# Kernel optimization log

Hardware: AMD Instinct MI355X
Metric: run time of the kernel (lower is better)

The kernel has to match this reference:

```python
import jax, jax.numpy as jnp
import numpy as np

N_TYPES = 4
N_PAIRS = N_TYPES * N_TYPES          # 16 (src_type, dst_type) pairs
N_GLOBAL_ET = 24                     # global edge event types
N_LOCAL_ET = 16                      # per-pair predictor output classes
D = 256                              # hidden dim
E = 262144                           # number of edges


def setup_inputs() -> dict:
    key = jax.random.key(0)
    ks = jax.random.split(key, 12)
    s = 0.05
    h_src = jax.random.normal(ks[0], (E, D), jnp.float32)
    h_dst = jax.random.normal(ks[1], (E, D), jnp.float32)
    src_type_idx = jax.random.randint(ks[2], (E,), 0, N_TYPES)
    dst_type_idx = jax.random.randint(ks[3], (E,), 0, N_TYPES)
    edge_type_classes = jax.random.randint(ks[4], (E,), 0, N_GLOBAL_ET)
    # decoder params: Linear(concat(h_src,h_dst)) -> D, split into two matrices
    W1 = jax.random.normal(ks[5], (D, D), jnp.float32) * s
    W2 = jax.random.normal(ks[6], (D, D), jnp.float32) * s
    b_dec = jnp.zeros((D,), jnp.float32)
    # per-(src,dst)-pair predictor heads, stacked
    W_pred = jax.random.normal(ks[7], (N_PAIRS, D, N_LOCAL_ET), jnp.float32) * s
    b_pred = jnp.zeros((N_PAIRS, N_LOCAL_ET), jnp.float32)
    # event_map[pair, global_edge_type] -> local class id
    event_map = jax.random.randint(ks[8], (N_PAIRS, N_GLOBAL_ET), 0, N_LOCAL_ET)
    return {
        'h_src': h_src, 'h_dst': h_dst,
        'W1': W1, 'W2': W2, 'b_dec': b_dec,
        'W_pred': W_pred, 'b_pred': b_pred,
        'src_type_idx': src_type_idx, 'dst_type_idx': dst_type_idx,
        'edge_type_classes': edge_type_classes, 'event_map': event_map,
        'inference': 0,
    }


def reference(h_src, h_dst, W1, W2, b_dec, W_pred, b_pred,
              src_type_idx, dst_type_idx, edge_type_classes, event_map,
              inference):
    # decoder: Linear(concat(h_src, h_dst)) -> D, ReLU
    h = jax.nn.relu(h_src @ W1 + h_dst @ W2 + b_dec)            # [E, D]
    pair = src_type_idx * N_TYPES + dst_type_idx                 # [E]
    # grouped per-pair linear heads: compute all heads, select per-edge head
    logits_all = jnp.einsum('ed,pdc->epc', h, W_pred) + b_pred   # [E, P, C]
    logits = jnp.take_along_axis(
        logits_all, pair[:, None, None], axis=1)[:, 0]           # [E, C]
    labels = event_map[pair, edge_type_classes]                  # [E]
    logp = jax.nn.log_softmax(logits, axis=-1)
    per_edge_loss = -jnp.take_along_axis(logp, labels[:, None], axis=1)[:, 0]
    # training path: per-group mean, then mean over non-empty groups
    sums = jax.ops.segment_sum(per_edge_loss, pair, num_segments=N_PAIRS)
    cnts = jax.ops.segment_sum(jnp.ones_like(per_edge_loss), pair,
                               num_segments=N_PAIRS)
    present = cnts > 0
    gmean = jnp.where(present, sums / jnp.maximum(cnts, 1.0), 0.0)
    loss = jnp.sum(gmean) / jnp.sum(present.astype(jnp.float32))
    return loss
```

## Files before the change

### kernel.cpp

```cpp
#include <hip/hip_runtime.h>
#include <stdint.h>

#define E_EDGES 262144
#define TILE_M 128
#define NBLK (E_EDGES / TILE_M)

typedef unsigned short ushort_t;
typedef __attribute__((ext_vector_type(8))) short short8;
typedef __attribute__((ext_vector_type(4))) float f32x4;

#define OFF_WT   0
#define OFF_WP   (512*256*2)
#define OFF_HIST (OFF_WP + 8*16*64*8*2)
#define OFF_SUMS (OFF_HIST + 64)

__device__ __forceinline__ ushort_t f2bf(float f) {
  union { float f; unsigned u; } c; c.f = f;
  unsigned r = c.u + 0x7fffu + ((c.u >> 16) & 1u);
  return (ushort_t)(r >> 16);
}

__device__ __forceinline__ void async_copy16(void* lds, const void* g) {
  __builtin_amdgcn_global_load_lds(
      (const __attribute__((address_space(1))) unsigned int*)g,
      (__attribute__((address_space(3))) unsigned int*)lds, 16, 0, 0);
}

__global__ __launch_bounds__(256) void prep_k(const float* __restrict__ W1,
    const float* __restrict__ W2, const float* __restrict__ Wp,
    char* __restrict__ ws) {
  const int i = blockIdx.x * 256 + threadIdx.x;
  if (i < 512 * 256) {
    ushort_t* Wt = (ushort_t*)(ws + OFF_WT);
    const int n = i >> 9, k = i & 511;
    const float v = (k < 256) ? W1[(k << 8) + n] : W2[((k - 256) << 8) + n];
    Wt[i] = f2bf(v);
  }
  if (i < 8 * 16 * 64 * 8) {
    ushort_t* Wpf = (ushort_t*)(ws + OFF_WP);
    const int jj = i & 7, l = (i >> 3) & 63, p = (i >> 9) & 15, s = i >> 13;
    const int k = s * 32 + (l >> 4) * 8 + jj, c = l & 15;
    Wpf[i] = f2bf(Wp[((p << 8) + k) * 16 + c]);
  }
  if (i < 16) {
    ((int*)(ws + OFF_HIST))[i] = 0;
    ((float*)(ws + OFF_SUMS))[i] = 0.f;
  }
}

__global__ __launch_bounds__(512, 4) void main_k(
    const float* __restrict__ h_src, const float* __restrict__ h_dst,
    const float* __restrict__ b_dec, const float* __restrict__ b_pred,
    const int* __restrict__ st, const int* __restrict__ dt,
    const int* __restrict__ etc_arr, const int* __restrict__ emap,
    char* __restrict__ ws) {
  const ushort_t* Wt = (const ushort_t*)(ws + OFF_WT);
  const short8* Wpf2 = (const short8*)(ws + OFF_WP);
  int* hist = (int*)(ws + OFF_HIST);
  float* sums = (float*)(ws + OFF_SUMS);

  const int tb = blockIdx.x * TILE_M;

  __shared__ __align__(16) char smem[65536];
  __shared__ float lsums[16];
  __shared__ int lcnts[16];
  ushort_t* A_buf0 = (ushort_t*)smem;
  ushort_t* A_buf1 = (ushort_t*)(smem + 10240);
  char* B_buf0 = smem + 20480;
  char* B_buf1 = smem + 36864;
  ushort_t* H_ls = (ushort_t*)smem;

  const int t = threadIdx.x;
  const int w = t >> 6, lane = t & 63;
  const int quad = lane >> 4, l15 = lane & 15;
  const int wm = w >> 2, wn = w & 3;

  const int arow = t >> 2, acg = t & 3;
  const int e_row = tb + arow;

  if (t < 16) { lsums[t] = 0.f; lcnts[t] = 0; }

  const f32x4 zero4 = {0.f, 0.f, 0.f, 0.f};
  f32x4 acc[4][4];
#pragma unroll
  for (int i = 0; i < 4; ++i)
#pragma unroll
    for (int j = 0; j < 4; ++j) acc[i][j] = zero4;

  auto stage_B = [&](int kt, char* Bb) {
#pragma unroll
    for (int ci = 0; ci < 2; ++ci) {
      const int chunk = w * 2 + ci;
      const int n = chunk * 16 + l15;
      const int k = kt * 32 + quad * 8;
      async_copy16(Bb + chunk * 1024, Wt + n * 512 + k);
    }
  };
  auto gather_A = [&](int kt, f32x4* fv) {
    const float* srcb = (kt < 8) ? h_src : h_dst;
    const f32x4* gp = (const f32x4*)(srcb + ((size_t)e_row << 8) + (kt & 7) * 32 + acg * 8);
    fv[0] = gp[0];
    fv[1] = gp[1];
  };
  auto conv_write = [&](const f32x4* fv, ushort_t* Ab) {
    union { ushort_t u[8]; short8 v; } pk;
#pragma unroll
    for (int q = 0; q < 2; ++q)
#pragma unroll
      for (int x = 0; x < 4; ++x) pk.u[q * 4 + x] = f2bf(fv[q][x]);
    *(short8*)(Ab + arow * 40 + acg * 8) = pk.v;
  };
  auto mma_step = [&](const ushort_t* Ab, const char* Bb) {
    short8 a[4];
#pragma unroll
    for (int i = 0; i < 4; ++i)
      a[i] = *(const short8*)(Ab + (wm * 64 + i * 16 + l15) * 40 + quad * 8);
#pragma unroll
    for (int j = 0; j < 4; ++j) {
      const short8 b = *(const short8*)(Bb + (wn * 4 + j) * 1024 + lane * 16);
#pragma unroll
      for (int i = 0; i < 4; ++i)
        acc[i][j] = __builtin_amdgcn_mfma_f32_16x16x32_bf16(a[i], b, acc[i][j], 0, 0, 0);
    }
  };

  f32x4 ga0[2], ga1[2];
  gather_A(0, ga0);
  __builtin_amdgcn_sched_barrier(0);
  stage_B(0, B_buf0);
  __builtin_amdgcn_sched_barrier(0);
  gather_A(1, ga1);
  __builtin_amdgcn_sched_barrier(0);
  conv_write(ga0, A_buf0);
  asm volatile("s_waitcnt vmcnt(2) lgkmcnt(0)" ::: "memory");
  __builtin_amdgcn_s_barrier();
  __builtin_amdgcn_sched_barrier(0);

#pragma unroll
  for (int kt = 0; kt < 15; ++kt) {
    ushort_t* Acur = (kt & 1) ? A_buf1 : A_buf0;
    ushort_t* Anxt = (kt & 1) ? A_buf0 : A_buf1;
    char* Bcur = (kt & 1) ? B_buf1 : B_buf0;
    char* Bnxt = (kt & 1) ? B_buf0 : B_buf1;
    f32x4* g_nxt = (kt & 1) ? ga0 : ga1;
    f32x4* g_new = (kt & 1) ? ga1 : ga0;

    stage_B(kt + 1, Bnxt);
    __builtin_amdgcn_sched_barrier(0);
    gather_A(kt + 2, g_new);
    __builtin_amdgcn_sched_barrier(0);
    mma_step(Acur, Bcur);
    asm volatile("s_waitcnt vmcnt(4)" ::: "memory");
    conv_write(g_nxt, Anxt);
    asm volatile("s_waitcnt vmcnt(2) lgkmcnt(0)" ::: "memory");
    __builtin_amdgcn_s_barrier();
    __builtin_amdgcn_sched_barrier(0);
  }
  mma_step(A_buf1, B_buf1);
  __syncthreads();

  float bj[4];
#pragma unroll
  for (int j = 0; j < 4; ++j) bj[j] = b_dec[wn * 64 + j * 16 + l15];
#pragma unroll
  for (int i = 0; i < 4; ++i)
#pragma unroll
    for (int j = 0; j < 4; ++j)
#pragma unroll
      for (int r = 0; r < 4; ++r) {
        const int row = wm * 64 + i * 16 + quad * 4 + r;
        const int col = wn * 64 + j * 16 + l15;
        float v = acc[i][j][r] + bj[j];
        v = fmaxf(v, 0.f);
        H_ls[row * 256 + (((col >> 3) ^ (row & 7)) << 3) + (col & 7)] = f2bf(v);
      }
  __syncthreads();

  f32x4 acc2[4][4];
#pragma unroll
  for (int i = 0; i < 4; ++i)
#pragma unroll
    for (int j = 0; j < 4; ++j) acc2[i][j] = zero4;
#pragma unroll
  for (int s = 0; s < 8; ++s) {
    short8 a[4], b[4];
#pragma unroll
    for (int x = 0; x < 4; ++x) {
      const int row = wm * 64 + x * 16 + l15;
      a[x] = *(const short8*)(H_ls + row * 256 + (((s * 4 + quad) ^ (row & 7)) << 3));
    }
#pragma unroll
    for (int j = 0; j < 4; ++j)
      b[j] = Wpf2[(s * 16 + wn * 4 + j) * 64 + lane];
#pragma unroll
    for (int x = 0; x < 4; ++x)
#pragma unroll
      for (int j = 0; j < 4; ++j)
        acc2[x][j] = __builtin_amdgcn_mfma_f32_16x16x32_bf16(a[x], b[j], acc2[x][j], 0, 0, 0);
  }

  float bpj[4];
#pragma unroll
  for (int j = 0; j < 4; ++j) bpj[j] = b_pred[(wn * 4 + j) * 16 + l15];
  float wsum[4] = {0.f, 0.f, 0.f, 0.f};
  int wcnt[4] = {0, 0, 0, 0};
#pragma unroll
  for (int i = 0; i < 4; ++i)
#pragma unroll
    for (int r = 0; r < 4; ++r) {
      const int row = wm * 64 + i * 16 + quad * 4 + r;
      const int e = tb + row;
      const int pe = st[e] * 4 + dt[e];
      float v = 0.f;
#pragma unroll
      for (int j = 0; j < 4; ++j) {
        const bool hit = (pe == wn * 4 + j);
        v = hit ? (acc2[i][j][r] + bpj[j]) : v;
      }
      float m = v;
#pragma unroll
      for (int o = 1; o < 16; o <<= 1) m = fmaxf(m, __shfl_xor(m, o, 16));
      float sm = __expf(v - m);
#pragma unroll
      for (int o = 1; o < 16; o <<= 1) sm += __shfl_xor(sm, o, 16);
      const int label = emap[pe * 24 + etc_arr[e]];
      const float vlab = __shfl(v, (lane & 48) + label, 64);
      const float loss = m + __logf(sm) - vlab;
#pragma unroll
      for (int j = 0; j < 4; ++j)
        if (pe == wn * 4 + j && l15 == 0) { wsum[j] += loss; wcnt[j] += 1; }
    }
  __syncthreads();
#pragma unroll
  for (int j = 0; j < 4; ++j) {
    float wv = wsum[j];
    int cv = wcnt[j];
    wv += __shfl_xor(wv, 16, 64);
    wv += __shfl_xor(wv, 32, 64);
    cv += __shfl_xor(cv, 16, 64);
    cv += __shfl_xor(cv, 32, 64);
    if (lane == 0 && cv > 0) {
      atomicAdd(&lsums[wn * 4 + j], wv);
      atomicAdd(&lcnts[wn * 4 + j], cv);
    }
  }
  __syncthreads();
  if (t < 16 && lcnts[t] > 0) {
    atomicAdd(&sums[t], lsums[t]);
    atomicAdd(&hist[t], lcnts[t]);
  }
}

__global__ void finalize_k(const char* __restrict__ ws, float* __restrict__ out) {
  const float* sums = (const float*)(ws + OFF_SUMS);
  const int* hist = (const int*)(ws + OFF_HIST);
  const int t = threadIdx.x;
  float g = 0.f, pr = 0.f;
  if (t < 16) {
    const int c = hist[t];
    if (c > 0) { g = sums[t] / (float)c; pr = 1.f; }
  }
#pragma unroll
  for (int o = 1; o < 16; o <<= 1) { g += __shfl_xor(g, o, 64); pr += __shfl_xor(pr, o, 64); }
  if (t == 0) out[0] = g / pr;
}

extern "C" void kernel_launch(void* const* d_in, const int* in_sizes, int n_in,
                              void* d_out, int out_size, void* d_ws, size_t ws_size,
                              hipStream_t stream) {
  const float* h_src  = (const float*)d_in[0];
  const float* h_dst  = (const float*)d_in[1];
  const float* W1     = (const float*)d_in[2];
  const float* W2     = (const float*)d_in[3];
  const float* b_dec  = (const float*)d_in[4];
  const float* W_pred = (const float*)d_in[5];
  const float* b_pred = (const float*)d_in[6];
  const int* st   = (const int*)d_in[7];
  const int* dt   = (const int*)d_in[8];
  const int* etc  = (const int*)d_in[9];
  const int* emap = (const int*)d_in[10];
  char* ws = (char*)d_ws;
  float* out = (float*)d_out;

  prep_k<<<512, 256, 0, stream>>>(W1, W2, W_pred, ws);
  main_k<<<NBLK, 512, 0, stream>>>(h_src, h_dst, b_dec, b_pred, st, dt, etc, emap, ws);
  finalize_k<<<1, 64, 0, stream>>>(ws, out);
}
```

Baseline: 612.3 us.

## Stage fp32 activations to LDS asynchronously and load weights straight into registers

```diff
diff --git a/kernel.cpp b/kernel.cpp
--- a/kernel.cpp
+++ b/kernel.cpp
@@ -18,6 +18,12 @@
   union { float f; unsigned u; } c; c.f = f;
   unsigned r = c.u + 0x7fffu + ((c.u >> 16) & 1u);
   return (ushort_t)(r >> 16);
+}
+
+__device__ __forceinline__ unsigned cvtpk_bf16(float lo, float hi) {
+  unsigned r;
+  asm("v_cvt_pk_bf16_f32 %0, %1, %2" : "=v"(r) : "v"(lo), "v"(hi));
+  return r;
 }
 
 __device__ __forceinline__ void async_copy16(void* lds, const void* g) {
@@ -64,10 +70,9 @@
   __shared__ __align__(16) char smem[65536];
   __shared__ float lsums[16];
   __shared__ int lcnts[16];
-  ushort_t* A_buf0 = (ushort_t*)smem;
-  ushort_t* A_buf1 = (ushort_t*)(smem + 10240);
-  char* B_buf0 = smem + 20480;
-  char* B_buf1 = smem + 36864;
+  char* const A_buf0 = smem;
+  char* const A_buf1 = smem + 16384;
+  char* const A_buf2 = smem + 32768;
   ushort_t* H_ls = (ushort_t*)smem;
 
   const int t = threadIdx.x;
@@ -75,9 +80,6 @@
   const int quad = lane >> 4, l15 = lane & 15;
   const int wm = w >> 2, wn = w & 3;
 
-  const int arow = t >> 2, acg = t & 3;
-  const int e_row = tb + arow;
-
   if (t < 16) { lsums[t] = 0.f; lcnts[t] = 0; }
 
   const f32x4 zero4 = {0.f, 0.f, 0.f, 0.f};
@@ -87,76 +89,75 @@
 #pragma unroll
     for (int j = 0; j < 4; ++j) acc[i][j] = zero4;
 
-  auto stage_B = [&](int kt, char* Bb) {
-#pragma unroll
-    for (int ci = 0; ci < 2; ++ci) {
-      const int chunk = w * 2 + ci;
-      const int n = chunk * 16 + l15;
-      const int k = kt * 32 + quad * 8;
-      async_copy16(Bb + chunk * 1024, Wt + n * 512 + k);
-    }
+  const int srow = t >> 3;
+  const int scol = ((t & 7) ^ (srow & 7)) * 4;
+  auto stage_A = [&](int kt, char* buf) {
+    const float* srcb = (kt < 8) ? h_src : h_dst;
+    const int kof = (kt & 7) * 32;
+    async_copy16(buf + t * 16,
+                 srcb + ((size_t)(tb + srow) << 8) + kof + scol);
+    async_copy16(buf + 8192 + t * 16,
+                 srcb + ((size_t)(tb + 64 + srow) << 8) + kof + scol);
   };
-  auto gather_A = [&](int kt, f32x4* fv) {
-    const float* srcb = (kt < 8) ? h_src : h_dst;
-    const f32x4* gp = (const f32x4*)(srcb + ((size_t)e_row << 8) + (kt & 7) * 32 + acg * 8);
-    fv[0] = gp[0];
-    fv[1] = gp[1];
+  auto load_B = [&](int kt, short8* breg) {
+#pragma unroll
+    for (int j = 0; j < 4; ++j)
+      breg[j] = *(const short8*)(Wt + (wn * 64 + j * 16 + l15) * 512 + kt * 32 + quad * 8);
   };
-  auto conv_write = [&](const f32x4* fv, ushort_t* Ab) {
-    union { ushort_t u[8]; short8 v; } pk;
-#pragma unroll
-    for (int q = 0; q < 2; ++q)
-#pragma unroll
-      for (int x = 0; x < 4; ++x) pk.u[q * 4 + x] = f2bf(fv[q][x]);
-    *(short8*)(Ab + arow * 40 + acg * 8) = pk.v;
+  const int c_lo = ((quad * 2) ^ (l15 & 7)) * 16;
+  const int c_hi = ((quad * 2 + 1) ^ (l15 & 7)) * 16;
+  auto mma_stage = [&](const char* Ab, const short8* breg) {
+    short8 a[4];
+#pragma unroll
+    for (int i = 0; i < 4; ++i) {
+      const int rbase = (wm * 64 + i * 16 + l15) * 128;
+      const f32x4 lo = *(const f32x4*)(Ab + rbase + c_lo);
+      const f32x4 hi = *(const f32x4*)(Ab + rbase + c_hi);
+      union { unsigned u[4]; short8 v; } pk;
+      pk.u[0] = cvtpk_bf16(lo[0], lo[1]);
+      pk.u[1] = cvtpk_bf16(lo[2], lo[3]);
+      pk.u[2] = cvtpk_bf16(hi[0], hi[1]);
+      pk.u[3] = cvtpk_bf16(hi[2], hi[3]);
+      a[i] = pk.v;
+    }
+#pragma unroll
+    for (int j = 0; j < 4; ++j)
+#pragma unroll
+      for (int i = 0; i < 4; ++i)
+        acc[i][j] = __builtin_amdgcn_mfma_f32_16x16x32_bf16(a[i], breg[j], acc[i][j], 0, 0, 0);
   };
-  auto mma_step = [&](const ushort_t* Ab, const char* Bb) {
-    short8 a[4];
-#pragma unroll
-    for (int i = 0; i < 4; ++i)
-      a[i] = *(const short8*)(Ab + (wm * 64 + i * 16 + l15) * 40 + quad * 8);
-#pragma unroll
-    for (int j = 0; j < 4; ++j) {
-      const short8 b = *(const short8*)(Bb + (wn * 4 + j) * 1024 + lane * 16);
-#pragma unroll
-      for (int i = 0; i < 4; ++i)
-        acc[i][j] = __builtin_amdgcn_mfma_f32_16x16x32_bf16(a[i], b, acc[i][j], 0, 0, 0);
-    }
-  };
-
-  f32x4 ga0[2], ga1[2];
-  gather_A(0, ga0);
-  __builtin_amdgcn_sched_barrier(0);
-  stage_B(0, B_buf0);
-  __builtin_amdgcn_sched_barrier(0);
-  gather_A(1, ga1);
-  __builtin_amdgcn_sched_barrier(0);
-  conv_write(ga0, A_buf0);
-  asm volatile("s_waitcnt vmcnt(2) lgkmcnt(0)" ::: "memory");
+
+  short8 breg[2][4];
+  char* const Abuf[3] = {A_buf0, A_buf1, A_buf2};
+
+  stage_A(0, A_buf0);
+  __builtin_amdgcn_sched_barrier(0);
+  load_B(0, breg[0]);
+  __builtin_amdgcn_sched_barrier(0);
+  stage_A(1, A_buf1);
+  __builtin_amdgcn_sched_barrier(0);
+  asm volatile("s_waitcnt vmcnt(2)" ::: "memory");
   __builtin_amdgcn_s_barrier();
   __builtin_amdgcn_sched_barrier(0);
 
 #pragma unroll
-  for (int kt = 0; kt < 15; ++kt) {
-    ushort_t* Acur = (kt & 1) ? A_buf1 : A_buf0;
-    ushort_t* Anxt = (kt & 1) ? A_buf0 : A_buf1;
-    char* Bcur = (kt & 1) ? B_buf1 : B_buf0;
-    char* Bnxt = (kt & 1) ? B_buf0 : B_buf1;
-    f32x4* g_nxt = (kt & 1) ? ga0 : ga1;
-    f32x4* g_new = (kt & 1) ? ga1 : ga0;
-
-    stage_B(kt + 1, Bnxt);
+  for (int kt = 0; kt < 14; ++kt) {
+    load_B(kt + 1, breg[(kt + 1) & 1]);
     __builtin_amdgcn_sched_barrier(0);
-    gather_A(kt + 2, g_new);
+    stage_A(kt + 2, Abuf[(kt + 2) % 3]);
     __builtin_amdgcn_sched_barrier(0);
-    mma_step(Acur, Bcur);
-    asm volatile("s_waitcnt vmcnt(4)" ::: "memory");
-    conv_write(g_nxt, Anxt);
-    asm volatile("s_waitcnt vmcnt(2) lgkmcnt(0)" ::: "memory");
+    mma_stage(Abuf[kt % 3], breg[kt & 1]);
+    asm volatile("s_waitcnt vmcnt(2)" ::: "memory");
     __builtin_amdgcn_s_barrier();
     __builtin_amdgcn_sched_barrier(0);
   }
-  mma_step(A_buf1, B_buf1);
+  load_B(15, breg[1]);
+  __builtin_amdgcn_sched_barrier(0);
+  mma_stage(A_buf2, breg[0]);
+  asm volatile("s_waitcnt vmcnt(0)" ::: "memory");
+  __builtin_amdgcn_s_barrier();
+  __builtin_amdgcn_sched_barrier(0);
+  mma_stage(A_buf0, breg[1]);
   __syncthreads();
 
   float bj[4];
```

Result: slower. 830.6 us (+35.6%).
